# Kernel tuning notes

Hardware: AMD Instinct MI355X
Metric: run time of the kernel (lower is better)

## Reference

```python
import jax, jax.numpy as jnp
import numpy as np

V, D, J = 1024, 1024, 1024  # num_outputs, predictor_dim, joiner_dim
B, U = 64, 512
NULL_INDEX = 0


def setup_inputs() -> dict:
    key = jax.random.key(0)
    ks = jax.random.split(key, 9)
    s = 0.02
    return {
        "y": jax.random.randint(ks[0], (B, U), 0, V, dtype=jnp.int64) if jax.config.jax_enable_x64 else jax.random.randint(ks[0], (B, U), 0, V, dtype=jnp.int32),
        "embed": jax.random.normal(ks[1], (V, D), jnp.float32) * s,
        "weight_ih": jax.random.normal(ks[2], (3 * D, D), jnp.float32) * s,
        "bias_ih": jax.random.normal(ks[3], (3 * D,), jnp.float32) * s,
        "weight_hh": jax.random.normal(ks[4], (3 * D, D), jnp.float32) * s,
        "bias_hh": jax.random.normal(ks[5], (3 * D,), jnp.float32) * s,
        "linear_w": jax.random.normal(ks[6], (J, D), jnp.float32) * s,
        "linear_b": jax.random.normal(ks[7], (J,), jnp.float32) * s,
        "initial_state": jax.random.normal(ks[8], (D,), jnp.float32),
    }


def reference(y, embed, weight_ih, bias_ih, weight_hh, bias_hh, linear_w, linear_b, initial_state):
    b, u_len = y.shape
    d = initial_state.shape[0]
    # Decoder input sequence: start symbol (NULL_INDEX=0) then the labels -> length U+1
    tokens = jnp.concatenate([jnp.full((b, 1), NULL_INDEX, dtype=y.dtype), y], axis=1)  # [B, U+1]
    x = embed[tokens]  # [B, U+1, D]
    # Precompute input-side gate pre-activations for all steps (batched GEMM)
    gx = jnp.einsum("bud,gd->bug", x, weight_ih) + bias_ih  # [B, U+1, 3D]
    h0 = jnp.broadcast_to(initial_state, (b, d))

    def step(h, gx_t):
        # PyTorch GRUCell: gates ordered (r, z, n)
        gh = h @ weight_hh.T + bias_hh  # [B, 3D]
        r = jax.nn.sigmoid(gx_t[:, :d] + gh[:, :d])
        z = jax.nn.sigmoid(gx_t[:, d:2 * d] + gh[:, d:2 * d])
        n = jnp.tanh(gx_t[:, 2 * d:] + r * gh[:, 2 * d:])
        h_new = (1.0 - z) * n + z * h
        return h_new, h_new

    _, hs = jax.lax.scan(step, h0, jnp.swapaxes(gx, 0, 1))  # hs: [U+1, B, D]
    out = jnp.einsum("ubd,jd->buj", hs, linear_w) + linear_b  # [B, U+1, J]
    return out
```

## Files before the change

kernel.cpp:

```cpp
#include <hip/hip_runtime.h>
#include <hip/hip_bf16.h>

typedef float f32x4 __attribute__((ext_vector_type(4)));
typedef short s16x8 __attribute__((ext_vector_type(8)));
typedef int   i32x4 __attribute__((ext_vector_type(4)));
typedef _Float16 h16x8 __attribute__((ext_vector_type(8)));

#define NV 1024
#define ND 1024
#define NJ 1024
#define NB 64
#define NU 512
#define NT 513
#define G3 3072
#define SLOT 65536
#define NWG 64
#define FSTRIDE 32
#define NFLAGS 256

static __device__ __forceinline__ unsigned short f2h(float f) {
  union { _Float16 h; unsigned short u; } x; x.h = (_Float16)f;
  return x.u;
}

static __device__ __forceinline__ void unswizzle(long e, int& r, int& k) {
  long blk = e >> 9; int l = (int)((e >> 3) & 63); int j = (int)(e & 7);
  r = (int)(blk >> 5) * 16 + (l & 15);
  k = ((int)(blk & 31)) * 32 + ((l >> 4) << 3) + j;
}

__global__ void predictor_prep(const float* __restrict__ whh, const float* __restrict__ wih,
                               const float* __restrict__ em, const float* __restrict__ lw,
                               const float* __restrict__ bih, const float* __restrict__ bhh,
                               const float* __restrict__ init,
                               unsigned short* __restrict__ wh_sw, unsigned short* __restrict__ wi_sw,
                               unsigned short* __restrict__ em_sw, unsigned short* __restrict__ lw_sw,
                               float* __restrict__ bias_sum, unsigned short* __restrict__ hs,
                               unsigned int* __restrict__ flags) {
  long e = (long)blockIdx.x * 256 + threadIdx.x;
  const long nbig = 3145728, nsm = 1048576;
  if (e < nbig) { int r, k; unswizzle(e, r, k); wh_sw[e] = f2h(whh[(long)r * 1024 + k]); return; }
  e -= nbig;
  if (e < nbig) { int r, k; unswizzle(e, r, k); wi_sw[e] = f2h(wih[(long)r * 1024 + k]); return; }
  e -= nbig;
  if (e < nsm) { int r, k; unswizzle(e, r, k); em_sw[e] = f2h(em[(long)r * 1024 + k]); return; }
  e -= nsm;
  if (e < nsm) { int r, k; unswizzle(e, r, k); lw_sw[e] = f2h(lw[(long)r * 1024 + k]); return; }
  e -= nsm;
  if (e < 65536) { int r, k; unswizzle(e, r, k); hs[e] = f2h(init[k]); return; }
  e -= 65536;
  if (e < 3072) { bias_sum[e] = bih[e] + bhh[e]; return; }
  e -= 3072;
  if (e < 8192) flags[e] = 0u;
}

__global__ __launch_bounds__(256) void predictor_gemm(
    const unsigned short* __restrict__ A, long a_chunk_stride,
    const unsigned short* __restrict__ Bw,
    const float* __restrict__ bias, float* __restrict__ out,
    int rowmul_i, int rowmul_c, int out_stride) {
  const int nt = blockIdx.x, chunk = blockIdx.y;
  const int tid = threadIdx.x, lane = tid & 63, wave = tid >> 6;
  const unsigned short* Ab = A + (long)chunk * a_chunk_stride + wave * 16384 + lane * 8;
  const unsigned short* Bb = Bw + (long)nt * 65536 + lane * 8;
  f32x4 a0 = {0,0,0,0}, a1 = {0,0,0,0}, a2 = {0,0,0,0}, a3 = {0,0,0,0};
#pragma unroll 4
  for (int kc = 0; kc < 32; ++kc) {
    h16x8 av = __builtin_bit_cast(h16x8, *(const s16x8*)(Ab + kc * 512));
    h16x8 w0 = __builtin_bit_cast(h16x8, *(const s16x8*)(Bb + kc * 512));
    h16x8 w1 = __builtin_bit_cast(h16x8, *(const s16x8*)(Bb + 16384 + kc * 512));
    h16x8 w2 = __builtin_bit_cast(h16x8, *(const s16x8*)(Bb + 32768 + kc * 512));
    h16x8 w3 = __builtin_bit_cast(h16x8, *(const s16x8*)(Bb + 49152 + kc * 512));
    a0 = __builtin_amdgcn_mfma_f32_16x16x32_f16(av, w0, a0, 0, 0, 0);
    a1 = __builtin_amdgcn_mfma_f32_16x16x32_f16(av, w1, a1, 0, 0, 0);
    a2 = __builtin_amdgcn_mfma_f32_16x16x32_f16(av, w2, a2, 0, 0, 0);
    a3 = __builtin_amdgcn_mfma_f32_16x16x32_f16(av, w3, a3, 0, 0, 0);
  }
  const int q = lane >> 4, nl = lane & 15, colbase = nt << 6;
#pragma unroll
  for (int j = 0; j < 4; ++j) {
    int il = (wave << 4) + (q << 2) + j;
    long row = (long)il * rowmul_i + (long)chunk * rowmul_c;
    float* orow = out + row * out_stride + colbase;
    orow[nl]      = a0[j] + bias[colbase + nl];
    orow[16 + nl] = a1[j] + bias[colbase + 16 + nl];
    orow[32 + nl] = a2[j] + bias[colbase + 32 + nl];
    orow[48 + nl] = a3[j] + bias[colbase + 48 + nl];
  }
}

#define PINSTAGE(CNT, B)                                                        \
  asm volatile("s_waitcnt vmcnt(" #CNT ")"                                      \
    : "+v"(hf[(B)*8+0]), "+v"(hf[(B)*8+1]), "+v"(hf[(B)*8+2]), "+v"(hf[(B)*8+3]), \
      "+v"(hf[(B)*8+4]), "+v"(hf[(B)*8+5]), "+v"(hf[(B)*8+6]), "+v"(hf[(B)*8+7]) :: "memory")

__global__ __launch_bounds__(256, 1) void predictor_rnn(
    const unsigned short* __restrict__ wh_sw, const float* __restrict__ gtab,
    const int* __restrict__ y, const float* __restrict__ init,
    unsigned short* __restrict__ hs, unsigned int* __restrict__ flags) {
  __shared__ float buf[4][3][4][64][4];
  __shared__ unsigned short tbuf[1024];
  const int wg = blockIdx.x, tid = threadIdx.x, lane = tid & 63, w = tid >> 6;
  const int q = lane >> 4, dloc = lane & 15, dg = (wg << 4) + dloc;

  h16x8 wrf[8], wzf[8], wnf[8];
#pragma unroll
  for (int i = 0; i < 8; ++i) {
    int kc = (w << 3) + i;
    wrf[i] = __builtin_bit_cast(h16x8, *(const s16x8*)(wh_sw + ((long)(      wg) << 14) + kc * 512 + lane * 8));
    wzf[i] = __builtin_bit_cast(h16x8, *(const s16x8*)(wh_sw + ((long)( 64 + wg) << 14) + kc * 512 + lane * 8));
    wnf[i] = __builtin_bit_cast(h16x8, *(const s16x8*)(wh_sw + ((long)(128 + wg) << 14) + kc * 512 + lane * 8));
  }
  float hreg[4];
#pragma unroll
  for (int j = 0; j < 4; ++j) hreg[j] = init[dg];

  for (int t = 1; t <= NT; ++t) {
    float gr[4], gz[4], gn[4];
#pragma unroll
    for (int j = 0; j < 4; ++j) {
      int b = (w << 4) + (q << 2) + j;
      int tok = (t == 1) ? 0 : y[b * NU + (t - 2)];
      const float* g = gtab + (long)tok * G3 + dg;
      asm volatile("global_load_dword %0, %1, off" : "=v"(gr[j]) : "v"(g) : "memory");
      asm volatile("global_load_dword %0, %1, off" : "=v"(gz[j]) : "v"(g + 1024) : "memory");
      asm volatile("global_load_dword %0, %1, off" : "=v"(gn[j]) : "v"(g + 2048) : "memory");
    }

    if (t > 1) {
      const unsigned int* fp = flags + (unsigned)((w << 6) + lane) * FSTRIDE;
      const unsigned int tm1 = (unsigned)(t - 1);
      for (;;) {
        unsigned int v;
        asm volatile("global_load_dword %0, %1, off sc1" : "=v"(v) : "v"(fp) : "memory");
        asm volatile("s_waitcnt vmcnt(0)" : "+v"(v) :: "memory");
        if (__all((int)(v >= tm1))) break;
        __builtin_amdgcn_s_sleep(2);
      }
    }
    asm volatile("s_waitcnt vmcnt(0)"
      : "+v"(gr[0]), "+v"(gr[1]), "+v"(gr[2]), "+v"(gr[3]),
        "+v"(gz[0]), "+v"(gz[1]), "+v"(gz[2]), "+v"(gz[3]),
        "+v"(gn[0]), "+v"(gn[1]), "+v"(gn[2]), "+v"(gn[3]) :: "memory");

    const unsigned short* hprev = hs + (long)(t - 1) * SLOT;
    unsigned short* hcur = hs + (long)t * SLOT;

    i32x4 hf[32];
#pragma unroll
    for (int bg = 0; bg < 4; ++bg)
#pragma unroll
      for (int i = 0; i < 8; ++i) {
        const unsigned short* a = hprev + bg * 16384 + ((w << 3) + i) * 512 + lane * 8;
        asm volatile("global_load_dwordx4 %0, %1, off sc1" : "=v"(hf[bg * 8 + i]) : "v"(a) : "memory");
      }
    f32x4 aR[4], aZ[4], aN[4];
#pragma unroll
    for (int bg = 0; bg < 4; ++bg) { aR[bg] = (f32x4){0,0,0,0}; aZ[bg] = (f32x4){0,0,0,0}; aN[bg] = (f32x4){0,0,0,0}; }
    {
      PINSTAGE(24, 0);
#pragma unroll
      for (int i = 0; i < 8; ++i) { h16x8 a = __builtin_bit_cast(h16x8, hf[0 * 8 + i]);
        aR[0] = __builtin_amdgcn_mfma_f32_16x16x32_f16(a, wrf[i], aR[0], 0, 0, 0);
        aZ[0] = __builtin_amdgcn_mfma_f32_16x16x32_f16(a, wzf[i], aZ[0], 0, 0, 0);
        aN[0] = __builtin_amdgcn_mfma_f32_16x16x32_f16(a, wnf[i], aN[0], 0, 0, 0); }
      PINSTAGE(16, 1);
#pragma unroll
      for (int i = 0; i < 8; ++i) { h16x8 a = __builtin_bit_cast(h16x8, hf[1 * 8 + i]);
        aR[1] = __builtin_amdgcn_mfma_f32_16x16x32_f16(a, wrf[i], aR[1], 0, 0, 0);
        aZ[1] = __builtin_amdgcn_mfma_f32_16x16x32_f16(a, wzf[i], aZ[1], 0, 0, 0);
        aN[1] = __builtin_amdgcn_mfma_f32_16x16x32_f16(a, wnf[i], aN[1], 0, 0, 0); }
      PINSTAGE(8, 2);
#pragma unroll
      for (int i = 0; i < 8; ++i) { h16x8 a = __builtin_bit_cast(h16x8, hf[2 * 8 + i]);
        aR[2] = __builtin_amdgcn_mfma_f32_16x16x32_f16(a, wrf[i], aR[2], 0, 0, 0);
        aZ[2] = __builtin_amdgcn_mfma_f32_16x16x32_f16(a, wzf[i], aZ[2], 0, 0, 0);
        aN[2] = __builtin_amdgcn_mfma_f32_16x16x32_f16(a, wnf[i], aN[2], 0, 0, 0); }
      PINSTAGE(0, 3);
#pragma unroll
      for (int i = 0; i < 8; ++i) { h16x8 a = __builtin_bit_cast(h16x8, hf[3 * 8 + i]);
        aR[3] = __builtin_amdgcn_mfma_f32_16x16x32_f16(a, wrf[i], aR[3], 0, 0, 0);
        aZ[3] = __builtin_amdgcn_mfma_f32_16x16x32_f16(a, wzf[i], aZ[3], 0, 0, 0);
        aN[3] = __builtin_amdgcn_mfma_f32_16x16x32_f16(a, wnf[i], aN[3], 0, 0, 0); }
    }

#pragma unroll
    for (int b2 = 0; b2 < 4; ++b2)
      if (b2 != w) {
        *(f32x4*)&buf[w][0][b2][lane][0] = aR[b2];
        *(f32x4*)&buf[w][1][b2][lane][0] = aZ[b2];
        *(f32x4*)&buf[w][2][b2][lane][0] = aN[b2];
      }
    __syncthreads();
    f32x4 sR = aR[w], sZ = aZ[w], sN = aN[w];
#pragma unroll
    for (int v = 0; v < 4; ++v)
      if (v != w) {
        sR += *(const f32x4*)&buf[v][0][w][lane][0];
        sZ += *(const f32x4*)&buf[v][1][w][lane][0];
        sN += *(const f32x4*)&buf[v][2][w][lane][0];
      }
    __syncthreads();

#pragma unroll
    for (int j = 0; j < 4; ++j) {
      float r = 1.f / (1.f + __expf(-(gr[j] + sR[j])));
      float z = 1.f / (1.f + __expf(-(gz[j] + sZ[j])));
      float np = gn[j] + r * sN[j];
      float e2 = __expf(-2.f * fabsf(np));
      float tn = (1.f - e2) / (1.f + e2);
      tn = np < 0.f ? -tn : tn;
      float hnew = (1.f - z) * tn + z * hreg[j];
      hreg[j] = hnew;
      tbuf[(w << 8) + ((((q << 2) + j) | ((dloc >> 3) << 4)) << 3) + (dloc & 7)] = f2h(hnew);
    }
    asm volatile("s_waitcnt lgkmcnt(0)" ::: "memory");

    {
      unsigned long long pv = *(const unsigned long long*)(tbuf + (w << 8) + lane * 4);
      unsigned short* gp = hcur + ((long)(w * 32 + (wg >> 1)) << 9) + ((wg & 1) << 8) + lane * 4;
      asm volatile("global_store_dwordx2 %0, %1, off sc1" :: "v"(gp), "v"(pv) : "memory");
      asm volatile("s_waitcnt vmcnt(0)" ::: "memory");
      if (lane == 0)
        __hip_atomic_store(&flags[((wg << 2) + w) * FSTRIDE], (unsigned)t,
                           __ATOMIC_RELAXED, __HIP_MEMORY_SCOPE_AGENT);
    }
  }
}

extern "C" void kernel_launch(void* const* d_in, const int* in_sizes, int n_in,
                              void* d_out, int out_size, void* d_ws, size_t ws_size,
                              hipStream_t stream) {
  const int*   y    = (const int*)d_in[0];
  const float* em   = (const float*)d_in[1];
  const float* wih  = (const float*)d_in[2];
  const float* bih  = (const float*)d_in[3];
  const float* whh  = (const float*)d_in[4];
  const float* bhh  = (const float*)d_in[5];
  const float* lw   = (const float*)d_in[6];
  const float* lb   = (const float*)d_in[7];
  const float* init = (const float*)d_in[8];
  float* out = (float*)d_out;

  char* ws = (char*)d_ws;
  size_t off = 0;
  auto alloc = [&](size_t n) { void* p = ws + off; off += (n + 255) & ~(size_t)255; return p; };
  unsigned short* wh_sw   = (unsigned short*)alloc(6291456);
  unsigned short* wi_sw   = (unsigned short*)alloc(6291456);
  unsigned short* em_sw   = (unsigned short*)alloc(2097152);
  unsigned short* lw_sw   = (unsigned short*)alloc(2097152);
  float*          gtab    = (float*)alloc(12582912);
  float*          bias_sum= (float*)alloc(12288);
  unsigned int*   flags   = (unsigned int*)alloc(32768);
  unsigned short* hs      = (unsigned short*)alloc(67371008UL);
  (void)ws_size; (void)in_sizes; (void)n_in; (void)out_size;

  predictor_prep<<<dim3(33068), dim3(256), 0, stream>>>(
      whh, wih, em, lw, bih, bhh, init, wh_sw, wi_sw, em_sw, lw_sw, bias_sum, hs, flags);
  predictor_gemm<<<dim3(48, 16), dim3(256), 0, stream>>>(
      em_sw, 65536L, wi_sw, bias_sum, gtab, 1, 64, 3072);
  predictor_rnn<<<dim3(NWG), dim3(256), 0, stream>>>(wh_sw, gtab, y, init, hs, flags);
  predictor_gemm<<<dim3(16, 513), dim3(256), 0, stream>>>(
      hs + 65536, 65536L, lw_sw, lb, out, 513, 1, 1024);
}
```

Measured before the change: 3.104 ms.

## Replace per-step flag polling with canary-based data validation in GRU recurrence

Removes the flag array and the store-then-flag handshake between workgroups. Instead, the prep kernel fills every hidden-state slot with a canary fp16 pattern (0x7FFF), and consumers reload each batch-group slice until no canary remains, so synchronisation rides on the data itself. This drops a full round trip per step (waiting for the store to complete before writing the flag, then polling the flag before loading h). In exchange, prep must write about 64MB of canary data, and correctness relies on the 16-byte stores being seen atomically and on real fp16 outputs never equalling the canary.

```diff
diff --git a/kernel.cpp b/kernel.cpp
--- a/kernel.cpp
+++ b/kernel.cpp
@@ -15,8 +15,7 @@
 #define G3 3072
 #define SLOT 65536
 #define NWG 64
-#define FSTRIDE 32
-#define NFLAGS 256
+#define CANARY 0x7FFF7FFFu
 
 static __device__ __forceinline__ unsigned short f2h(float f) {
   union { _Float16 h; unsigned short u; } x; x.h = (_Float16)f;
@@ -35,8 +34,7 @@
                                const float* __restrict__ init,
                                unsigned short* __restrict__ wh_sw, unsigned short* __restrict__ wi_sw,
                                unsigned short* __restrict__ em_sw, unsigned short* __restrict__ lw_sw,
-                               float* __restrict__ bias_sum, unsigned short* __restrict__ hs,
-                               unsigned int* __restrict__ flags) {
+                               float* __restrict__ bias_sum, unsigned short* __restrict__ hs) {
   long e = (long)blockIdx.x * 256 + threadIdx.x;
   const long nbig = 3145728, nsm = 1048576;
   if (e < nbig) { int r, k; unswizzle(e, r, k); wh_sw[e] = f2h(whh[(long)r * 1024 + k]); return; }
@@ -51,7 +49,11 @@
   e -= 65536;
   if (e < 3072) { bias_sum[e] = bih[e] + bhh[e]; return; }
   e -= 3072;
-  if (e < 8192) flags[e] = 0u;
+  if (e < 4202496) {
+    s16x8 c = { (short)0x7FFF, (short)0x7FFF, (short)0x7FFF, (short)0x7FFF,
+                (short)0x7FFF, (short)0x7FFF, (short)0x7FFF, (short)0x7FFF };
+    *(s16x8*)(hs + 65536 + e * 8) = c;
+  }
 }
 
 __global__ __launch_bounds__(256) void predictor_gemm(
@@ -94,10 +96,33 @@
     : "+v"(hf[(B)*8+0]), "+v"(hf[(B)*8+1]), "+v"(hf[(B)*8+2]), "+v"(hf[(B)*8+3]), \
       "+v"(hf[(B)*8+4]), "+v"(hf[(B)*8+5]), "+v"(hf[(B)*8+6]), "+v"(hf[(B)*8+7]) :: "memory")
 
+#define PVALID(B, CNT)                                                          \
+  {                                                                             \
+    PINSTAGE(CNT, B);                                                           \
+    for (;;) {                                                                  \
+      int ok = 1;                                                               \
+      _Pragma("unroll")                                                         \
+      for (int i = 0; i < 8; ++i) {                                             \
+        i32x4 v = hf[(B)*8 + i];                                                \
+        ok &= (v[0] != (int)CANARY) & (v[1] != (int)CANARY) &                   \
+              (v[2] != (int)CANARY) & (v[3] != (int)CANARY);                    \
+      }                                                                         \
+      if (__all(ok)) break;                                                     \
+      __builtin_amdgcn_s_sleep(1);                                              \
+      _Pragma("unroll")                                                         \
+      for (int i = 0; i < 8; ++i) {                                             \
+        const unsigned short* a2_ = hprev + (B)*16384 + ((w<<3)+i)*512 + lane*8;\
+        asm volatile("global_load_dwordx4 %0, %1, off sc1"                      \
+                     : "=v"(hf[(B)*8+i]) : "v"(a2_) : "memory");                \
+      }                                                                         \
+      PINSTAGE(0, B);                                                           \
+    }                                                                           \
+  }
+
 __global__ __launch_bounds__(256, 1) void predictor_rnn(
     const unsigned short* __restrict__ wh_sw, const float* __restrict__ gtab,
     const int* __restrict__ y, const float* __restrict__ init,
-    unsigned short* __restrict__ hs, unsigned int* __restrict__ flags) {
+    unsigned short* __restrict__ hs) {
   __shared__ float buf[4][3][4][64][4];
   __shared__ unsigned short tbuf[1024];
   const int wg = blockIdx.x, tid = threadIdx.x, lane = tid & 63, w = tid >> 6;
@@ -127,22 +152,6 @@
       asm volatile("global_load_dword %0, %1, off" : "=v"(gn[j]) : "v"(g + 2048) : "memory");
     }
 
-    if (t > 1) {
-      const unsigned int* fp = flags + (unsigned)((w << 6) + lane) * FSTRIDE;
-      const unsigned int tm1 = (unsigned)(t - 1);
-      for (;;) {
-        unsigned int v;
-        asm volatile("global_load_dword %0, %1, off sc1" : "=v"(v) : "v"(fp) : "memory");
-        asm volatile("s_waitcnt vmcnt(0)" : "+v"(v) :: "memory");
-        if (__all((int)(v >= tm1))) break;
-        __builtin_amdgcn_s_sleep(2);
-      }
-    }
-    asm volatile("s_waitcnt vmcnt(0)"
-      : "+v"(gr[0]), "+v"(gr[1]), "+v"(gr[2]), "+v"(gr[3]),
-        "+v"(gz[0]), "+v"(gz[1]), "+v"(gz[2]), "+v"(gz[3]),
-        "+v"(gn[0]), "+v"(gn[1]), "+v"(gn[2]), "+v"(gn[3]) :: "memory");
-
     const unsigned short* hprev = hs + (long)(t - 1) * SLOT;
     unsigned short* hcur = hs + (long)t * SLOT;
 
@@ -157,32 +166,36 @@
     f32x4 aR[4], aZ[4], aN[4];
 #pragma unroll
     for (int bg = 0; bg < 4; ++bg) { aR[bg] = (f32x4){0,0,0,0}; aZ[bg] = (f32x4){0,0,0,0}; aN[bg] = (f32x4){0,0,0,0}; }
-    {
-      PINSTAGE(24, 0);
-#pragma unroll
-      for (int i = 0; i < 8; ++i) { h16x8 a = __builtin_bit_cast(h16x8, hf[0 * 8 + i]);
-        aR[0] = __builtin_amdgcn_mfma_f32_16x16x32_f16(a, wrf[i], aR[0], 0, 0, 0);
-        aZ[0] = __builtin_amdgcn_mfma_f32_16x16x32_f16(a, wzf[i], aZ[0], 0, 0, 0);
-        aN[0] = __builtin_amdgcn_mfma_f32_16x16x32_f16(a, wnf[i], aN[0], 0, 0, 0); }
-      PINSTAGE(16, 1);
-#pragma unroll
-      for (int i = 0; i < 8; ++i) { h16x8 a = __builtin_bit_cast(h16x8, hf[1 * 8 + i]);
-        aR[1] = __builtin_amdgcn_mfma_f32_16x16x32_f16(a, wrf[i], aR[1], 0, 0, 0);
-        aZ[1] = __builtin_amdgcn_mfma_f32_16x16x32_f16(a, wzf[i], aZ[1], 0, 0, 0);
-        aN[1] = __builtin_amdgcn_mfma_f32_16x16x32_f16(a, wnf[i], aN[1], 0, 0, 0); }
-      PINSTAGE(8, 2);
-#pragma unroll
-      for (int i = 0; i < 8; ++i) { h16x8 a = __builtin_bit_cast(h16x8, hf[2 * 8 + i]);
-        aR[2] = __builtin_amdgcn_mfma_f32_16x16x32_f16(a, wrf[i], aR[2], 0, 0, 0);
-        aZ[2] = __builtin_amdgcn_mfma_f32_16x16x32_f16(a, wzf[i], aZ[2], 0, 0, 0);
-        aN[2] = __builtin_amdgcn_mfma_f32_16x16x32_f16(a, wnf[i], aN[2], 0, 0, 0); }
-      PINSTAGE(0, 3);
-#pragma unroll
-      for (int i = 0; i < 8; ++i) { h16x8 a = __builtin_bit_cast(h16x8, hf[3 * 8 + i]);
-        aR[3] = __builtin_amdgcn_mfma_f32_16x16x32_f16(a, wrf[i], aR[3], 0, 0, 0);
-        aZ[3] = __builtin_amdgcn_mfma_f32_16x16x32_f16(a, wzf[i], aZ[3], 0, 0, 0);
-        aN[3] = __builtin_amdgcn_mfma_f32_16x16x32_f16(a, wnf[i], aN[3], 0, 0, 0); }
-    }
+
+    PVALID(0, 24);
+#pragma unroll
+    for (int i = 0; i < 8; ++i) { h16x8 a = __builtin_bit_cast(h16x8, hf[0 * 8 + i]);
+      aR[0] = __builtin_amdgcn_mfma_f32_16x16x32_f16(a, wrf[i], aR[0], 0, 0, 0);
+      aZ[0] = __builtin_amdgcn_mfma_f32_16x16x32_f16(a, wzf[i], aZ[0], 0, 0, 0);
+      aN[0] = __builtin_amdgcn_mfma_f32_16x16x32_f16(a, wnf[i], aN[0], 0, 0, 0); }
+    PVALID(1, 16);
+#pragma unroll
+    for (int i = 0; i < 8; ++i) { h16x8 a = __builtin_bit_cast(h16x8, hf[1 * 8 + i]);
+      aR[1] = __builtin_amdgcn_mfma_f32_16x16x32_f16(a, wrf[i], aR[1], 0, 0, 0);
+      aZ[1] = __builtin_amdgcn_mfma_f32_16x16x32_f16(a, wzf[i], aZ[1], 0, 0, 0);
+      aN[1] = __builtin_amdgcn_mfma_f32_16x16x32_f16(a, wnf[i], aN[1], 0, 0, 0); }
+    PVALID(2, 8);
+#pragma unroll
+    for (int i = 0; i < 8; ++i) { h16x8 a = __builtin_bit_cast(h16x8, hf[2 * 8 + i]);
+      aR[2] = __builtin_amdgcn_mfma_f32_16x16x32_f16(a, wrf[i], aR[2], 0, 0, 0);
+      aZ[2] = __builtin_amdgcn_mfma_f32_16x16x32_f16(a, wzf[i], aZ[2], 0, 0, 0);
+      aN[2] = __builtin_amdgcn_mfma_f32_16x16x32_f16(a, wnf[i], aN[2], 0, 0, 0); }
+    PVALID(3, 0);
+#pragma unroll
+    for (int i = 0; i < 8; ++i) { h16x8 a = __builtin_bit_cast(h16x8, hf[3 * 8 + i]);
+      aR[3] = __builtin_amdgcn_mfma_f32_16x16x32_f16(a, wrf[i], aR[3], 0, 0, 0);
+      aZ[3] = __builtin_amdgcn_mfma_f32_16x16x32_f16(a, wzf[i], aZ[3], 0, 0, 0);
+      aN[3] = __builtin_amdgcn_mfma_f32_16x16x32_f16(a, wnf[i], aN[3], 0, 0, 0); }
+
+    asm volatile("s_waitcnt vmcnt(0)"
+      : "+v"(gr[0]), "+v"(gr[1]), "+v"(gr[2]), "+v"(gr[3]),
+        "+v"(gz[0]), "+v"(gz[1]), "+v"(gz[2]), "+v"(gz[3]),
+        "+v"(gn[0]), "+v"(gn[1]), "+v"(gn[2]), "+v"(gn[3]) :: "memory");
 
 #pragma unroll
     for (int b2 = 0; b2 < 4; ++b2)
@@ -220,10 +233,6 @@
       unsigned long long pv = *(const unsigned long long*)(tbuf + (w << 8) + lane * 4);
       unsigned short* gp = hcur + ((long)(w * 32 + (wg >> 1)) << 9) + ((wg & 1) << 8) + lane * 4;
       asm volatile("global_store_dwordx2 %0, %1, off sc1" :: "v"(gp), "v"(pv) : "memory");
-      asm volatile("s_waitcnt vmcnt(0)" ::: "memory");
-      if (lane == 0)
-        __hip_atomic_store(&flags[((wg << 2) + w) * FSTRIDE], (unsigned)t,
-                           __ATOMIC_RELAXED, __HIP_MEMORY_SCOPE_AGENT);
     }
   }
 }
@@ -251,15 +260,14 @@
   unsigned short* lw_sw   = (unsigned short*)alloc(2097152);
   float*          gtab    = (float*)alloc(12582912);
   float*          bias_sum= (float*)alloc(12288);
-  unsigned int*   flags   = (unsigned int*)alloc(32768);
   unsigned short* hs      = (unsigned short*)alloc(67371008UL);
   (void)ws_size; (void)in_sizes; (void)n_in; (void)out_size;
 
-  predictor_prep<<<dim3(33068), dim3(256), 0, stream>>>(
-      whh, wih, em, lw, bih, bhh, init, wh_sw, wi_sw, em_sw, lw_sw, bias_sum, hs, flags);
+  predictor_prep<<<dim3(49452), dim3(256), 0, stream>>>(
+      whh, wih, em, lw, bih, bhh, init, wh_sw, wi_sw, em_sw, lw_sw, bias_sum, hs);
   predictor_gemm<<<dim3(48, 16), dim3(256), 0, stream>>>(
       em_sw, 65536L, wi_sw, bias_sum, gtab, 1, 64, 3072);
-  predictor_rnn<<<dim3(NWG), dim3(256), 0, stream>>>(wh_sw, gtab, y, init, hs, flags);
+  predictor_rnn<<<dim3(NWG), dim3(256), 0, stream>>>(wh_sw, gtab, y, init, hs);
   predictor_gemm<<<dim3(16, 513), dim3(256), 0, stream>>>(
       hs + 65536, 65536L, lw_sw, lb, out, 513, 1, 1024);
 }
```

Result: slower. 3.425 ms (+10.4%).
